# Performance work log

Hardware: AMD Instinct MI355X
Metric: run time of the kernel (lower is better)

## Reference

```python
import jax, jax.numpy as jnp
import numpy as np

NUM_HEADS = 8

def setup_inputs() -> dict:
    key = jax.random.key(0)
    ks = jax.random.split(key, 12)
    B, C, H, W = 4, 256, 64, 64
    QK = 256
    NSP = 256
    x = jax.random.normal(ks[0], (B, C, H, W), dtype=jnp.float32)
    affinity_matrix = jax.random.uniform(ks[1], (B, NSP, H * W), dtype=jnp.float32)
    norm_w = 1.0 + 0.02 * jax.random.normal(ks[2], (C,), dtype=jnp.float32)
    norm_b = 0.02 * jax.random.normal(ks[3], (C,), dtype=jnp.float32)
    Wq = 0.02 * jax.random.normal(ks[4], (QK, C), dtype=jnp.float32)
    Wk = 0.02 * jax.random.normal(ks[5], (QK, C), dtype=jnp.float32)
    Wv = 0.02 * jax.random.normal(ks[6], (C, C), dtype=jnp.float32)
    Wsp = 0.02 * jax.random.normal(ks[7], (QK, C), dtype=jnp.float32)
    lepe_w = 0.02 * jax.random.normal(ks[8], (C, 1, 3, 3), dtype=jnp.float32)  # depthwise OIHW
    lepe_b = 0.02 * jax.random.normal(ks[9], (C,), dtype=jnp.float32)
    return {"x": x, "affinity_matrix": affinity_matrix, "norm_w": norm_w,
            "norm_b": norm_b, "Wq": Wq, "Wk": Wk, "Wv": Wv, "Wsp": Wsp,
            "lepe_w": lepe_w, "lepe_b": lepe_b, "num_spixels": NSP}


def _layernorm2d(x, w, b, eps=1e-6):
    # LayerNorm over channel dim of NCHW input
    xp = x.transpose(0, 2, 3, 1)  # B,H,W,C
    mu = xp.mean(-1, keepdims=True)
    var = ((xp - mu) ** 2).mean(-1, keepdims=True)
    xn = (xp - mu) * jax.lax.rsqrt(var + eps) * w + b
    return xn.transpose(0, 3, 1, 2)


def _sgca(x, affinity_matrix, norm_w, norm_b, Wq, Wk, Wv, Wsp, lepe_w, lepe_b, num_spixels):
    B, C, H, W = x.shape
    HW = H * W
    h = NUM_HEADS
    qk_dim = Wq.shape[0]
    dqk = qk_dim // h
    dv = C // h
    scale = (C // h) ** -0.5

    xn = _layernorm2d(x, norm_w, norm_b)

    # superpixel aggregation: b (hw) c
    x_flat = xn.reshape(B, C, HW).transpose(0, 2, 1)  # B,HW,C
    stoken = jnp.einsum('bmn,bnc->bmc', affinity_matrix, x_flat)
    stoken = stoken / (affinity_matrix.sum(-1, keepdims=True) + 1e-16)  # B,nsp,C

    # sp projection -> B,h,dqk,nsp
    st = jnp.einsum('bmc,qc->bmq', stoken, Wsp).transpose(0, 2, 1)
    st = st.reshape(B, h, dqk, num_spixels)

    # 1x1 conv projections
    q = jnp.einsum('oc,bchw->bohw', Wq, xn).reshape(B, h, dqk, HW)
    k = jnp.einsum('oc,bchw->bohw', Wk, xn).reshape(B, h, dqk, HW)
    vx = jnp.einsum('oc,bchw->bohw', Wv, xn)  # B,C,H,W
    v = vx.reshape(B, h, dv, HW)

    # LePE: depthwise 3x3 conv on v(x)
    lepe = jax.lax.conv_general_dilated(
        vx, lepe_w, window_strides=(1, 1), padding=((1, 1), (1, 1)),
        feature_group_count=C, dimension_numbers=('NCHW', 'OIHW', 'NCHW'))
    lepe = lepe + lepe_b[None, :, None, None]
    # faithful to original: [B,C,HW] -> permute -> [B,HW,C] -> reshape B,C,H,W
    lepe = lepe.reshape(B, C, HW).transpose(0, 2, 1).reshape(B, C, H, W)

    # stage 1: k^T @ stoken, softmax over HW axis
    s_attn = jnp.einsum('bhdn,bhdm->bhnm', k, st) * scale  # B,h,HW,nsp
    s_attn = jax.nn.softmax(s_attn, axis=-2)
    s_out = jnp.einsum('bhdn,bhnm->bhdm', v, s_attn)  # B,h,dv,nsp

    # stage 2: stoken^T @ q, softmax over nsp axis
    x_attn = jnp.einsum('bhdm,bhdn->bhmn', st, q) * scale  # B,h,nsp,HW
    x_attn = jax.nn.softmax(x_attn, axis=-2)
    x_out = jnp.einsum('bhdm,bhmn->bhdn', s_out, x_attn).reshape(B, C, H, W)

    return x_out + lepe


def reference(x, affinity_matrix, norm_w, norm_b, Wq, Wk, Wv, Wsp, lepe_w, lepe_b, num_spixels):
    return _sgca(x, affinity_matrix, norm_w, norm_b, Wq, Wk, Wv, Wsp, lepe_w, lepe_b, num_spixels)
```

## Files before the change

kernel.cpp:

```cpp
#include <hip/hip_runtime.h>
#include <hip/hip_bf16.h>

#define BATCH 4
#define CCH   256
#define HWHW  4096
#define NSP   256
#define NHEAD 8
#define SCALE 0.17677669529663689f
#define PLANE 1048576L

typedef short bf16x8 __attribute__((ext_vector_type(8)));
typedef short bf16x4 __attribute__((ext_vector_type(4)));
typedef float f32x4  __attribute__((ext_vector_type(4)));

__device__ __forceinline__ short f2bs(float f) {
    __hip_bfloat16 h = __float2bfloat16(f);
    return *(short*)&h;
}
__device__ __forceinline__ bf16x8 cvt8(float4 a, float4 b) {
    bf16x8 p;
    p[0] = f2bs(a.x); p[1] = f2bs(a.y); p[2] = f2bs(a.z); p[3] = f2bs(a.w);
    p[4] = f2bs(b.x); p[5] = f2bs(b.y); p[6] = f2bs(b.z); p[7] = f2bs(b.w);
    return p;
}

__global__ __launch_bounds__(512)
void ln_fused_kernel(const float* __restrict__ x, const float* __restrict__ w,
                     const float* __restrict__ bb,
                     const float* __restrict__ Wq, const float* __restrict__ Wk,
                     const float* __restrict__ Wv, const float* __restrict__ Wsp,
                     __hip_bfloat16* __restrict__ xn_cn,
                     __hip_bfloat16* __restrict__ xn_nc,
                     __hip_bfloat16* __restrict__ wbf)
{
    __shared__ float ps[32][64], pss[32][64];
    __shared__ float mus[64], rstds[64];
    __shared__ float wls[256], bls[256];
    int blk = blockIdx.x;
    int t = threadIdx.x;
    if (blk >= 256) {
        int sel = blk - 256;
        const float* src = (sel == 0) ? Wq : (sel == 1) ? Wk : (sel == 2) ? Wv : Wsp;
        __hip_bfloat16* dst = wbf + sel * 65536;
        for (int i = t * 4; i < 65536; i += 2048) {
            float4 f = *(const float4*)(src + i);
            __hip_bfloat16 p[4];
            p[0] = __float2bfloat16(f.x); p[1] = __float2bfloat16(f.y);
            p[2] = __float2bfloat16(f.z); p[3] = __float2bfloat16(f.w);
            *(int2*)(dst + i) = *(int2*)p;
        }
        return;
    }
    int b = blk >> 6;
    int n0 = (blk & 63) * 64;
    int pg = t & 15;
    int cq = t >> 4;
    if (t < 256) { wls[t] = w[t]; bls[t] = bb[t]; }

    const float* xp = x + ((long)(b * CCH + cq * 8)) * HWHW + n0 + pg * 4;
    float4 v[8];
#pragma unroll
    for (int i = 0; i < 8; ++i) v[i] = *(const float4*)(xp + (long)i * HWHW);
    float4 s = {0.f,0.f,0.f,0.f}, ss = {0.f,0.f,0.f,0.f};
#pragma unroll
    for (int i = 0; i < 8; ++i) {
        s.x += v[i].x; s.y += v[i].y; s.z += v[i].z; s.w += v[i].w;
        ss.x += v[i].x * v[i].x; ss.y += v[i].y * v[i].y;
        ss.z += v[i].z * v[i].z; ss.w += v[i].w * v[i].w;
    }
    *(float4*)&ps[cq][pg * 4]  = s;
    *(float4*)&pss[cq][pg * 4] = ss;
    __syncthreads();
    if (t < 64) {
        float S = 0.f, SS = 0.f;
#pragma unroll
        for (int q = 0; q < 32; ++q) { S += ps[q][t]; SS += pss[q][t]; }
        float mu = S * (1.f / 256.f);
        float var = SS * (1.f / 256.f) - mu * mu;
        mus[t] = mu; rstds[t] = rsqrtf(var + 1e-6f);
    }
    __syncthreads();
    float4 mu4 = *(float4*)&mus[pg * 4];
    float4 rs4 = *(float4*)&rstds[pg * 4];

    bf16x8 pk[4];
#pragma unroll
    for (int i = 0; i < 8; ++i) {
        int c = cq * 8 + i;
        float wc = wls[c], bc = bls[c];
        short h0 = f2bs((v[i].x - mu4.x) * rs4.x * wc + bc);
        short h1 = f2bs((v[i].y - mu4.y) * rs4.y * wc + bc);
        short h2 = f2bs((v[i].z - mu4.z) * rs4.z * wc + bc);
        short h3 = f2bs((v[i].w - mu4.w) * rs4.w * wc + bc);
        pk[0][i] = h0; pk[1][i] = h1; pk[2][i] = h2; pk[3][i] = h3;
        bf16x4 q; q[0] = h0; q[1] = h1; q[2] = h2; q[3] = h3;
        *(bf16x4*)(xn_cn + ((long)(b * CCH + c)) * HWHW + n0 + pg * 4) = q;
    }
#pragma unroll
    for (int j = 0; j < 4; ++j)
        *(bf16x8*)(xn_nc + ((long)b * HWHW + n0 + pg * 4 + j) * CCH + cq * 8) = pk[j];
}

template <int OUTK, bool AF32, bool ROWSUM, bool ASUM8>
__device__ __forceinline__ void gemm_body(
    const void* __restrict__ Av, const __hip_bfloat16* __restrict__ B,
    void* __restrict__ Cptr, int bx, int by, int bz,
    int N, int K, int kChunk, int kShift,
    long aStrideZ, long bStrideZ, long cStrideZ,
    float* __restrict__ rsPart,
    __hip_bfloat16* __restrict__ Asm, __hip_bfloat16* __restrict__ Bsm,
    float* __restrict__ rsl)
{
    int z = bz;
    int b = z >> kShift;
    int ch = z & ((1 << kShift) - 1);
    int t = threadIdx.x;
    int lane = t & 63, w = t >> 6;
    int l15 = lane & 15, quad = lane >> 4;
    int Mt = by * 64, Nt = bx * 64;

    if (ASUM8 && t < 64) {
        float s = 0.f;
#pragma unroll
        for (int pl = 0; pl < 8; ++pl) s += rsPart[((b * 8 + pl) << 8) + Mt + t];
        rsl[t] = s;
    }

    long aOff = (long)b * aStrideZ + (long)ch * kChunk
        + (long)(Mt + w * 16 + l15) * K + quad * 8;
    const __hip_bfloat16* aSrcH = (const __hip_bfloat16*)Av + aOff;
    const float*          aSrcF = (const float*)Av + aOff;
    const __hip_bfloat16* bSrc = B + (long)b * bStrideZ + (long)ch * kChunk
        + (long)(Nt + w * 16 + l15) * K + quad * 8;
    __hip_bfloat16* aDst = &Asm[t * 8];
    __hip_bfloat16* bDst = &Bsm[t * 8];

    f32x4 acc00 = {0.f,0.f,0.f,0.f}, acc01 = acc00, acc10 = acc00, acc11 = acc00;
    f32x4 rs0 = acc00, rs1 = acc00;
    bf16x8 onesf;
    { short o = (l15 == 0) ? (short)0x3F80 : (short)0;
      onesf = bf16x8{o, o, o, o, o, o, o, o}; }
    int wm = (w & 1) * 2, wn = (w >> 1) * 2;

    int4 aReg; float4 fA0, fA1;
    if (AF32) { fA0 = *(const float4*)aSrcF; fA1 = *(const float4*)(aSrcF + 4); }
    else if (!ASUM8) aReg = *(const int4*)aSrcH;
    int4 bReg = *(const int4*)bSrc;
    for (int k0 = 0; k0 < kChunk; k0 += 32) {
        if (ASUM8) {
            float4 s0 = {0.f,0.f,0.f,0.f}, s1 = {0.f,0.f,0.f,0.f};
#pragma unroll
            for (int pl = 0; pl < 8; ++pl) {
                const float* p = aSrcF + (long)pl * 65536 + k0;
                float4 u0 = *(const float4*)p, u1 = *(const float4*)(p + 4);
                s0.x += u0.x; s0.y += u0.y; s0.z += u0.z; s0.w += u0.w;
                s1.x += u1.x; s1.y += u1.y; s1.z += u1.z; s1.w += u1.w;
            }
            *(bf16x8*)aDst = cvt8(s0, s1);
        } else if (AF32) *(bf16x8*)aDst = cvt8(fA0, fA1);
        else             *(int4*)aDst = aReg;
        *(int4*)bDst = bReg;
        __syncthreads();
        if (k0 + 32 < kChunk) {
            bSrc += 32;
            bReg = *(const int4*)bSrc;
            if (AF32) { aSrcF += 32; fA0 = *(const float4*)aSrcF; fA1 = *(const float4*)(aSrcF + 4); }
            else if (!ASUM8) { aSrcH += 32; aReg = *(const int4*)aSrcH; }
        }
        bf16x8 a0 = ((const bf16x8*)Asm)[wm * 64 + lane];
        bf16x8 a1 = ((const bf16x8*)Asm)[(wm + 1) * 64 + lane];
        bf16x8 b0 = ((const bf16x8*)Bsm)[wn * 64 + lane];
        bf16x8 b1 = ((const bf16x8*)Bsm)[(wn + 1) * 64 + lane];
        acc00 = __builtin_amdgcn_mfma_f32_16x16x32_bf16(a0, b0, acc00, 0, 0, 0);
        acc01 = __builtin_amdgcn_mfma_f32_16x16x32_bf16(a0, b1, acc01, 0, 0, 0);
        acc10 = __builtin_amdgcn_mfma_f32_16x16x32_bf16(a1, b0, acc10, 0, 0, 0);
        acc11 = __builtin_amdgcn_mfma_f32_16x16x32_bf16(a1, b1, acc11, 0, 0, 0);
        if (ROWSUM) {
            rs0 = __builtin_amdgcn_mfma_f32_16x16x32_bf16(a0, onesf, rs0, 0, 0, 0);
            rs1 = __builtin_amdgcn_mfma_f32_16x16x32_bf16(a1, onesf, rs1, 0, 0, 0);
        }
        __syncthreads();
    }
    if (ROWSUM && bx == 0 && (w >> 1) == 0 && l15 == 0) {
#pragma unroll
        for (int r = 0; r < 4; ++r) {
            rsPart[(long)z * 256 + Mt + wm * 16 + quad * 4 + r]       = rs0[r];
            rsPart[(long)z * 256 + Mt + (wm + 1) * 16 + quad * 4 + r] = rs1[r];
        }
    }
    f32x4 accs[2][2] = {{acc00, acc01}, {acc10, acc11}};
#pragma unroll
    for (int i = 0; i < 2; ++i)
#pragma unroll
        for (int j = 0; j < 2; ++j)
#pragma unroll
            for (int r = 0; r < 4; ++r) {
                int m = Mt + (wm + i) * 16 + quad * 4 + r;
                int n = Nt + (wn + j) * 16 + l15;
                float val = accs[i][j][r];
                if (ASUM8) val /= (rsl[m - Mt] + 1e-16f);
                long off = (long)z * cStrideZ + (long)m * N + n;
                if (OUTK == 0) ((float*)Cptr)[off] = val;
                else ((__hip_bfloat16*)Cptr)[off] = __float2bfloat16(val);
            }
}

__global__ __launch_bounds__(256)
void mega1_kernel(const float* __restrict__ aff,
                  const __hip_bfloat16* __restrict__ xn_cn,
                  const __hip_bfloat16* __restrict__ xn_nc,
                  const __hip_bfloat16* __restrict__ wbf,
                  __hip_bfloat16* __restrict__ qk_nc,
                  __hip_bfloat16* __restrict__ v_cn,
                  float* __restrict__ stoken_part,
                  float* __restrict__ rs_part)
{
    __shared__ __hip_bfloat16 Asm[2048];
    __shared__ __hip_bfloat16 Bsm[2048];
    int blk = blockIdx.x;
    if (blk < 512) {
        int i = blk;
        gemm_body<0, true, true, false>(aff, xn_cn, stoken_part,
            i & 3, (i >> 2) & 3, i >> 4, 256, 4096, 512, 3,
            PLANE, PLANE, 65536L, rs_part, Asm, Bsm, nullptr);
    } else if (blk < 2560) {
        int i = blk - 512;
        gemm_body<1, false, false, false>(xn_nc, wbf, qk_nc,
            i & 7, (i >> 3) & 63, i >> 9, 512, 256, 256, 0,
            PLANE, 0L, 2 * PLANE, nullptr, Asm, Bsm, nullptr);
    } else {
        int i = blk - 2560;
        gemm_body<1, false, false, false>(wbf + 2 * 65536, xn_nc, v_cn,
            i & 63, (i >> 6) & 3, i >> 8, 4096, 256, 256, 0,
            0L, PLANE, PLANE, nullptr, Asm, Bsm, nullptr);
    }
}

__global__ __launch_bounds__(256)
void stmd_kernel(const float* __restrict__ part,
                 const __hip_bfloat16* __restrict__ wsp,
                 __hip_bfloat16* __restrict__ st_md,
                 float* __restrict__ rs_part)
{
    __shared__ __hip_bfloat16 Asm[2048];
    __shared__ __hip_bfloat16 Bsm[2048];
    __shared__ float rsl[64];
    int i = blockIdx.x;
    gemm_body<1, false, false, true>(part, wsp, st_md,
        i & 3, (i >> 2) & 3, i >> 4, 256, 256, 256, 0,
        524288L, 0L, 65536L, rs_part, Asm, Bsm, rsl);
}

__device__ __forceinline__
void stage1_dev(char* smem, int chunk, int bh,
                const __hip_bfloat16* __restrict__ qk_nc,
                const __hip_bfloat16* __restrict__ v_cn,
                const __hip_bfloat16* __restrict__ st_md,
                __hip_bfloat16* __restrict__ opart)
{
    __hip_bfloat16* Es  = (__hip_bfloat16*)smem;
    __hip_bfloat16* sts = (__hip_bfloat16*)(smem + 36864);
    const int b = bh >> 3, h = bh & 7;
    const int t = threadIdx.x, lane = t & 63, w = t >> 6;
    const int l15 = lane & 15, quad = lane >> 4;
    const int n0 = chunk * 256;

    {
        const int4* src = (const int4*)(st_md + ((long)(b * 256 + t)) * 256 + h * 32);
        int4* dst = (int4*)&sts[t * 40];
        dst[0] = src[0]; dst[1] = src[1]; dst[2] = src[2]; dst[3] = src[3];
    }
    __syncthreads();
    bf16x8 afrag[16];
#pragma unroll
    for (int mt = 0; mt < 16; ++mt)
        afrag[mt] = *(const bf16x8*)&sts[(mt * 16 + l15) * 40 + quad * 8];
    bf16x8 onesf;
    { short o = (l15 == 0) ? (short)0x3F80 : (short)0;
      onesf = bf16x8{o, o, o, o, o, o, o, o}; }

    f32x4 occ[4][3];
#pragma unroll
    for (int i = 0; i < 4; ++i)
#pragma unroll
        for (int j = 0; j < 3; ++j) occ[i][j] = f32x4{0.f,0.f,0.f,0.f};

    for (int sub = 0; sub < 4; ++sub) {
        const int nbase = n0 + sub * 64;
        bf16x8 kf = *(const bf16x8*)(qk_nc + ((long)b * 4096 + nbase + 16 * w + l15) * 512 + 256 + h * 32 + quad * 8);
#pragma unroll
        for (int mt = 0; mt < 16; ++mt) {
            f32x4 s = __builtin_amdgcn_mfma_f32_16x16x32_bf16(afrag[mt], kf, f32x4{0.f,0.f,0.f,0.f}, 0, 0, 0);
#pragma unroll
            for (int r = 0; r < 4; ++r)
                Es[(mt * 16 + quad * 4 + r) * 72 + 16 * w + l15] =
                    __float2bfloat16(__expf(s[r] * SCALE));
        }
        __syncthreads();
#pragma unroll
        for (int ks = 0; ks < 2; ++ks) {
            bf16x8 bf0 = *(const bf16x8*)(v_cn + ((long)(b * 256 + h * 32 + l15)) * 4096 + nbase + ks * 32 + quad * 8);
            bf16x8 bf1 = *(const bf16x8*)(v_cn + ((long)(b * 256 + h * 32 + 16 + l15)) * 4096 + nbase + ks * 32 + quad * 8);
#pragma unroll
            for (int mi = 0; mi < 4; ++mi) {
                bf16x8 af = *(const bf16x8*)&Es[(64 * w + mi * 16 + l15) * 72 + ks * 32 + quad * 8];
                occ[mi][0] = __builtin_amdgcn_mfma_f32_16x16x32_bf16(af, bf0, occ[mi][0], 0, 0, 0);
                occ[mi][1] = __builtin_amdgcn_mfma_f32_16x16x32_bf16(af, bf1, occ[mi][1], 0, 0, 0);
                occ[mi][2] = __builtin_amdgcn_mfma_f32_16x16x32_bf16(af, onesf, occ[mi][2], 0, 0, 0);
            }
        }
        __syncthreads();
    }
    __hip_bfloat16* tb = Es;
#pragma unroll
    for (int mi = 0; mi < 4; ++mi)
#pragma unroll
        for (int jt = 0; jt < 3; ++jt) {
            if (jt == 2 && l15 != 0) continue;
            int col = jt * 16 + l15;
#pragma unroll
            for (int r = 0; r < 4; ++r) {
                int m = 64 * w + mi * 16 + quad * 4 + r;
                tb[col * 264 + m] = __float2bfloat16(occ[mi][jt][r]);
            }
        }
    __syncthreads();
    int* og = (int*)(opart) + (long)(chunk * 32 + bh) * 4224;
    const int* tbi = (const int*)tb;
#pragma unroll
    for (int i = 0; i < 17; ++i) {
        int idx = t + i * 256;
        if (idx < 4224) {
            int row = idx >> 7, off = idx & 127;
            og[idx] = tbi[row * 132 + off];
        }
    }
}

__device__ __forceinline__
void lepe_dev(char* smem, int bx, int cy, int b,
              const __hip_bfloat16* __restrict__ v_cn,
              const float* __restrict__ lw, const float* __restrict__ lb,
              __hip_bfloat16* __restrict__ lepe_cn)
{
    __hip_bfloat16* in_t    = (__hip_bfloat16*)smem;
    __hip_bfloat16* tile_bf = (__hip_bfloat16*)(smem + 24576);
    float* wls = (float*)(smem + 41472);
    float* bls = (float*)(smem + 42624);
    const int c0 = cy * 32;
    const int t = threadIdx.x;
    const int n0 = bx * 256, r0 = bx * 4;

    for (int i = t; i < 288; i += 256) wls[i] = lw[c0 * 9 + i];
    if (t < 32)  bls[t] = lb[c0 + t];
#pragma unroll
    for (int i = 0; i < 6; ++i) {
        int vi = t + i * 256;
        int ch = vi / 48;
        int off = (vi % 48) * 8;
        int g = (r0 - 1) * 64 + off;
        int4 val = {0, 0, 0, 0};
        if ((unsigned)g < 4096u)
            val = *(const int4*)(v_cn + (((long)(b * CCH + c0 + ch)) << 12) + g);
        *(int4*)&in_t[ch * 384 + off] = val;
    }
    __syncthreads();

    const int lane = t & 63, w = t >> 6;
#pragma unroll
    for (int i = 0; i < 8; ++i) {
        int ch = w * 8 + i;
        float cr[6], lf[6], rf[6];
#pragma unroll
        for (int rr = 0; rr < 6; ++rr) {
            cr[rr] = (float)in_t[ch * 384 + rr * 64 + lane];
            float lv = __shfl_up(cr[rr], 1);
            float rv = __shfl_down(cr[rr], 1);
            lf[rr] = (lane == 0) ? 0.f : lv;
            rf[rr] = (lane == 63) ? 0.f : rv;
        }
        float w0 = wls[ch*9+0], w1 = wls[ch*9+1], w2 = wls[ch*9+2];
        float w3 = wls[ch*9+3], w4 = wls[ch*9+4], w5 = wls[ch*9+5];
        float w6 = wls[ch*9+6], w7 = wls[ch*9+7], w8 = wls[ch*9+8];
        float bias = bls[ch];
#pragma unroll
        for (int r = 0; r < 4; ++r) {
            float acc = bias
                + lf[r]   * w0 + cr[r]   * w1 + rf[r]   * w2
                + lf[r+1] * w3 + cr[r+1] * w4 + rf[r+1] * w5
                + lf[r+2] * w6 + cr[r+2] * w7 + rf[r+2] * w8;
            tile_bf[(r * 64 + lane) * 33 + ch] = __float2bfloat16(acc);
        }
    }
    __syncthreads();
#pragma unroll
    for (int i = 0; i < 32; ++i) {
        int idx = t + i * 256;
        int nl = idx >> 5, cj = idx & 31;
        int sp = n0 + nl;
        lepe_cn[((long)(b * CCH + (sp >> 4)) << 12) + (nl & 15) * 256 + c0 + cj] =
            tile_bf[nl * 33 + cj];
    }
}

__global__ __launch_bounds__(256)
void mega2_kernel(const __hip_bfloat16* __restrict__ qk_nc,
                  const __hip_bfloat16* __restrict__ v_cn,
                  const __hip_bfloat16* __restrict__ st_md,
                  __hip_bfloat16* __restrict__ opart,
                  const float* __restrict__ lw, const float* __restrict__ lb,
                  __hip_bfloat16* __restrict__ lepe_cn)
{
    __shared__ __align__(16) char smem[57344];
    int blk = blockIdx.x;
    if (blk < 512) {
        stage1_dev(smem, blk & 15, blk >> 4, qk_nc, v_cn, st_md, opart);
    } else {
        int j = blk - 512;
        lepe_dev(smem, j & 15, (j >> 4) & 7, j >> 7, v_cn, lw, lb, lepe_cn);
    }
}

__global__ __launch_bounds__(256)
void merge1_kernel(const __hip_bfloat16* __restrict__ opart, __hip_bfloat16* __restrict__ sout)
{
    int t = blockIdx.x * 256 + threadIdx.x;
    int m = t & 255;
    int d = (t >> 8) & 31;
    int bh = t >> 13;
    float num = 0.f, den = 0.f;
    for (int ch = 0; ch < 16; ++ch) {
        long base = (long)((ch * 32 + bh) * 33) * 256 + m;
        num += (float)opart[base + (long)d * 256];
        den += (float)opart[base + 32 * 256];
    }
    sout[(long)bh * 8192 + d * 256 + m] = __float2bfloat16(num / den);
}

__global__ __launch_bounds__(256)
void stage2_mfma(const __hip_bfloat16* __restrict__ qk_nc,
                 const __hip_bfloat16* __restrict__ st_md,
                 const __hip_bfloat16* __restrict__ sout_bf,
                 const __hip_bfloat16* __restrict__ lepe_cn,
                 float* __restrict__ out)
{
    __shared__ __hip_bfloat16 Es2[64 * 264];
    __shared__ __hip_bfloat16 sts[256 * 40];
    __shared__ __hip_bfloat16 sos[32 * 264];
    __shared__ float o_t[32 * 68];
    const int chunk = blockIdx.x, bh = blockIdx.y;
    const int b = bh >> 3, h = bh & 7;
    const int t = threadIdx.x, lane = t & 63, w = t >> 6;
    const int l15 = lane & 15, quad = lane >> 4;
    const int n0 = chunk * 256;

    {
        const int4* src = (const int4*)(st_md + ((long)(b * 256 + t)) * 256 + h * 32);
        int4* dst = (int4*)&sts[t * 40];
        dst[0] = src[0]; dst[1] = src[1]; dst[2] = src[2]; dst[3] = src[3];
    }
    {
        int row = t >> 3, seg = t & 7;
        const int4* src = (const int4*)(sout_bf + (long)bh * 8192 + row * 256 + seg * 32);
        int4* dst = (int4*)&sos[row * 264 + seg * 32];
        dst[0] = src[0]; dst[1] = src[1]; dst[2] = src[2]; dst[3] = src[3];
    }
    __syncthreads();
    bf16x8 stfrag[4];
#pragma unroll
    for (int mt = 0; mt < 4; ++mt)
        stfrag[mt] = *(const bf16x8*)&sts[(64 * w + mt * 16 + l15) * 40 + quad * 8];
    bf16x8 onesf;
    { short o = (l15 == 0) ? (short)0x3F80 : (short)0;
      onesf = bf16x8{o, o, o, o, o, o, o, o}; }

    for (int sub = 0; sub < 4; ++sub) {
        const int nbase = n0 + sub * 64;
#pragma unroll
        for (int nt = 0; nt < 4; ++nt) {
            bf16x8 qf = *(const bf16x8*)(qk_nc + ((long)b * 4096 + nbase + nt * 16 + l15) * 512 + h * 32 + quad * 8);
#pragma unroll
            for (int mt = 0; mt < 4; ++mt) {
                f32x4 s = __builtin_amdgcn_mfma_f32_16x16x32_bf16(qf, stfrag[mt], f32x4{0.f,0.f,0.f,0.f}, 0, 0, 0);
#pragma unroll
                for (int r = 0; r < 4; ++r)
                    Es2[(nt * 16 + quad * 4 + r) * 264 + 64 * w + mt * 16 + l15] =
                        __float2bfloat16(__expf(s[r] * SCALE));
            }
        }
        __syncthreads();
        f32x4 o0 = {0.f,0.f,0.f,0.f}, o1 = o0, o2 = o0;
#pragma unroll
        for (int ks = 0; ks < 8; ++ks) {
            bf16x8 af = *(const bf16x8*)&Es2[(16 * w + l15) * 264 + ks * 32 + quad * 8];
            bf16x8 b0 = *(const bf16x8*)&sos[(l15) * 264 + ks * 32 + quad * 8];
            bf16x8 b1 = *(const bf16x8*)&sos[(16 + l15) * 264 + ks * 32 + quad * 8];
            o0 = __builtin_amdgcn_mfma_f32_16x16x32_bf16(af, b0, o0, 0, 0, 0);
            o1 = __builtin_amdgcn_mfma_f32_16x16x32_bf16(af, b1, o1, 0, 0, 0);
            o2 = __builtin_amdgcn_mfma_f32_16x16x32_bf16(af, onesf, o2, 0, 0, 0);
        }
        __syncthreads();
#pragma unroll
        for (int r = 0; r < 4; ++r) {
            float den = __shfl(o2[r], lane & 48);
            float inv = 1.f / den;
            o_t[(l15) * 68 + 16 * w + quad * 4 + r]      = o0[r] * inv;
            o_t[(16 + l15) * 68 + 16 * w + quad * 4 + r] = o1[r] * inv;
        }
        __syncthreads();
        {
            int row = t >> 3, coff = (t & 7) * 8;
            long gb = ((long)(b * 256 + h * 32 + row)) * 4096 + nbase + coff;
            int4 lp4 = *(const int4*)(lepe_cn + gb);
            const __hip_bfloat16* lp = (const __hip_bfloat16*)&lp4;
            const float* sp = &o_t[row * 68 + coff];
            float4 r0, r1;
            r0.x = sp[0] + (float)lp[0]; r0.y = sp[1] + (float)lp[1];
            r0.z = sp[2] + (float)lp[2]; r0.w = sp[3] + (float)lp[3];
            r1.x = sp[4] + (float)lp[4]; r1.y = sp[5] + (float)lp[5];
            r1.z = sp[6] + (float)lp[6]; r1.w = sp[7] + (float)lp[7];
            *(float4*)(out + gb)     = r0;
            *(float4*)(out + gb + 4) = r1;
        }
        __syncthreads();
    }
}

extern "C" void kernel_launch(void* const* d_in, const int* in_sizes, int n_in,
                              void* d_out, int out_size, void* d_ws, size_t ws_size,
                              hipStream_t stream)
{
    const float* x    = (const float*)d_in[0];
    const float* aff  = (const float*)d_in[1];
    const float* nw   = (const float*)d_in[2];
    const float* nb   = (const float*)d_in[3];
    const float* Wq   = (const float*)d_in[4];
    const float* Wk   = (const float*)d_in[5];
    const float* Wv   = (const float*)d_in[6];
    const float* Wsp  = (const float*)d_in[7];
    const float* lw   = (const float*)d_in[8];
    const float* lb   = (const float*)d_in[9];
    float* out = (float*)d_out;

    float* ws = (float*)d_ws;
    const long P = PLANE;
    __hip_bfloat16* qk_nc  = (__hip_bfloat16*)(ws);
    __hip_bfloat16* v_cn   = (__hip_bfloat16*)(ws + 4 * P);
    __hip_bfloat16* xn_cn  = (__hip_bfloat16*)(ws + 6 * P);
    __hip_bfloat16* xn_nc  = (__hip_bfloat16*)(ws + 8 * P);
    __hip_bfloat16* lepe_cn= (__hip_bfloat16*)(ws + 10 * P);
    float* stoken_part = ws + 14 * P;
    __hip_bfloat16* opart = (__hip_bfloat16*)(ws + 16 * P);
    float* tail        = ws + 16 * P + 2162688;
    __hip_bfloat16* wbf       = (__hip_bfloat16*)tail;
    __hip_bfloat16* st_md     = (__hip_bfloat16*)(tail + 262144);
    __hip_bfloat16* sout_bf   = (__hip_bfloat16*)(tail + 393216);
    float* rs_part = tail + 525312;

    ln_fused_kernel<<<260, 512, 0, stream>>>(x, nw, nb, Wq, Wk, Wv, Wsp,
                                             xn_cn, xn_nc, wbf);
    mega1_kernel<<<3584, 256, 0, stream>>>(aff, xn_cn, xn_nc, wbf,
                                           qk_nc, v_cn, stoken_part, rs_part);
    stmd_kernel<<<64, 256, 0, stream>>>(stoken_part, wbf + 3 * 65536, st_md, rs_part);
    mega2_kernel<<<1024, 256, 0, stream>>>(qk_nc, v_cn, st_md, opart, lw, lb, lepe_cn);
    merge1_kernel<<<1024, 256, 0, stream>>>(opart, sout_bf);
    stage2_mfma<<<dim3(16, 32), 256, 0, stream>>>(qk_nc, st_md, sout_bf, lepe_cn, out);
}
```

Measured before the change: 212.3 us.

## Widen GEMM tiles, use direct global-to-LDS loads, double K step

The shared GEMM body now processes 64 K elements per barrier pair instead of 32, and loads bf16 operands with global_load_lds so they bypass registers. The affinity-aggregation GEMM now has each block compute four 64-column tiles (NTL=4), which reuses the fp32-to-bf16 converted affinity rows and cuts its block count from 512 to 128. The aim is fewer barriers, less register staging and less redundant conversion of the affinity matrix. In exchange LDS use per block rises to about 40 KB and the affinity GEMM has far fewer blocks, which may lower occupancy and parallelism.

After: 208.0 us. 1.02x faster.

```diff
diff --git a/kernel.cpp b/kernel.cpp
--- a/kernel.cpp
+++ b/kernel.cpp
@@ -22,6 +22,12 @@
     p[0] = f2bs(a.x); p[1] = f2bs(a.y); p[2] = f2bs(a.z); p[3] = f2bs(a.w);
     p[4] = f2bs(b.x); p[5] = f2bs(b.y); p[6] = f2bs(b.z); p[7] = f2bs(b.w);
     return p;
+}
+__device__ __forceinline__ void gll16(const __hip_bfloat16* g, __hip_bfloat16* l) {
+    __builtin_amdgcn_global_load_lds(
+        (const __attribute__((address_space(1))) unsigned int*)(const void*)g,
+        (__attribute__((address_space(3))) unsigned int*)(void*)l,
+        16, 0, 0);
 }
 
 __global__ __launch_bounds__(512)
@@ -101,7 +107,7 @@
         *(bf16x8*)(xn_nc + ((long)b * HWHW + n0 + pg * 4 + j) * CCH + cq * 8) = pk[j];
 }
 
-template <int OUTK, bool AF32, bool ROWSUM, bool ASUM8>
+template <int OUTK, int ASTAGE, bool ROWSUM, int NTL>
 __device__ __forceinline__ void gemm_body(
     const void* __restrict__ Av, const __hip_bfloat16* __restrict__ B,
     void* __restrict__ Cptr, int bx, int by, int bz,
@@ -117,9 +123,9 @@
     int t = threadIdx.x;
     int lane = t & 63, w = t >> 6;
     int l15 = lane & 15, quad = lane >> 4;
-    int Mt = by * 64, Nt = bx * 64;
-
-    if (ASUM8 && t < 64) {
+    int Mt = by * 64, Nt = bx * 64 * NTL;
+
+    if (ASTAGE == 2 && t < 64) {
         float s = 0.f;
 #pragma unroll
         for (int pl = 0; pl < 8; ++pl) s += rsPart[((b * 8 + pl) << 8) + Mt + t];
@@ -132,52 +138,78 @@
     const float*          aSrcF = (const float*)Av + aOff;
     const __hip_bfloat16* bSrc = B + (long)b * bStrideZ + (long)ch * kChunk
         + (long)(Nt + w * 16 + l15) * K + quad * 8;
-    __hip_bfloat16* aDst = &Asm[t * 8];
-    __hip_bfloat16* bDst = &Bsm[t * 8];
-
-    f32x4 acc00 = {0.f,0.f,0.f,0.f}, acc01 = acc00, acc10 = acc00, acc11 = acc00;
-    f32x4 rs0 = acc00, rs1 = acc00;
+
+    f32x4 acc[NTL][2][2];
+#pragma unroll
+    for (int nt = 0; nt < NTL; ++nt)
+#pragma unroll
+        for (int i = 0; i < 2; ++i)
+#pragma unroll
+            for (int j = 0; j < 2; ++j) acc[nt][i][j] = f32x4{0.f,0.f,0.f,0.f};
+    f32x4 rs0 = {0.f,0.f,0.f,0.f}, rs1 = rs0;
     bf16x8 onesf;
     { short o = (l15 == 0) ? (short)0x3F80 : (short)0;
       onesf = bf16x8{o, o, o, o, o, o, o, o}; }
     int wm = (w & 1) * 2, wn = (w >> 1) * 2;
 
-    int4 aReg; float4 fA0, fA1;
-    if (AF32) { fA0 = *(const float4*)aSrcF; fA1 = *(const float4*)(aSrcF + 4); }
-    else if (!ASUM8) aReg = *(const int4*)aSrcH;
-    int4 bReg = *(const int4*)bSrc;
-    for (int k0 = 0; k0 < kChunk; k0 += 32) {
-        if (ASUM8) {
-            float4 s0 = {0.f,0.f,0.f,0.f}, s1 = {0.f,0.f,0.f,0.f};
-#pragma unroll
-            for (int pl = 0; pl < 8; ++pl) {
-                const float* p = aSrcF + (long)pl * 65536 + k0;
-                float4 u0 = *(const float4*)p, u1 = *(const float4*)(p + 4);
-                s0.x += u0.x; s0.y += u0.y; s0.z += u0.z; s0.w += u0.w;
-                s1.x += u1.x; s1.y += u1.y; s1.z += u1.z; s1.w += u1.w;
+    float4 pf0, pf1, pf2, pf3;
+    if (ASTAGE == 1) {
+        pf0 = *(const float4*)(aSrcF);      pf1 = *(const float4*)(aSrcF + 4);
+        pf2 = *(const float4*)(aSrcF + 32); pf3 = *(const float4*)(aSrcF + 36);
+    }
+
+    const bf16x8* AsmU = (const bf16x8*)Asm;
+    const bf16x8* BsmU = (const bf16x8*)Bsm;
+
+    for (int k0 = 0; k0 < kChunk; k0 += 64) {
+        if (ASTAGE == 0) {
+            gll16(aSrcH + k0,      Asm + w * 512);
+            gll16(aSrcH + k0 + 32, Asm + 2048 + w * 512);
+        } else if (ASTAGE == 1) {
+            *(bf16x8*)&Asm[t * 8]        = cvt8(pf0, pf1);
+            *(bf16x8*)&Asm[2048 + t * 8] = cvt8(pf2, pf3);
+        } else {
+#pragma unroll
+            for (int kh = 0; kh < 2; ++kh) {
+                float4 s0 = {0.f,0.f,0.f,0.f}, s1 = {0.f,0.f,0.f,0.f};
+#pragma unroll
+                for (int pl = 0; pl < 8; ++pl) {
+                    const float* p = aSrcF + (long)pl * 65536 + k0 + kh * 32;
+                    float4 u0 = *(const float4*)p, u1 = *(const float4*)(p + 4);
+                    s0.x += u0.x; s0.y += u0.y; s0.z += u0.z; s0.w += u0.w;
+                    s1.x += u1.x; s1.y += u1.y; s1.z += u1.z; s1.w += u1.w;
+                }
+                *(bf16x8*)&Asm[kh * 2048 + t * 8] = cvt8(s0, s1);
             }
-            *(bf16x8*)aDst = cvt8(s0, s1);
-        } else if (AF32) *(bf16x8*)aDst = cvt8(fA0, fA1);
-        else             *(int4*)aDst = aReg;
-        *(int4*)bDst = bReg;
-        __syncthreads();
-        if (k0 + 32 < kChunk) {
-            bSrc += 32;
-            bReg = *(const int4*)bSrc;
-            if (AF32) { aSrcF += 32; fA0 = *(const float4*)aSrcF; fA1 = *(const float4*)(aSrcF + 4); }
-            else if (!ASUM8) { aSrcH += 32; aReg = *(const int4*)aSrcH; }
-        }
-        bf16x8 a0 = ((const bf16x8*)Asm)[wm * 64 + lane];
-        bf16x8 a1 = ((const bf16x8*)Asm)[(wm + 1) * 64 + lane];
-        bf16x8 b0 = ((const bf16x8*)Bsm)[wn * 64 + lane];
-        bf16x8 b1 = ((const bf16x8*)Bsm)[(wn + 1) * 64 + lane];
-        acc00 = __builtin_amdgcn_mfma_f32_16x16x32_bf16(a0, b0, acc00, 0, 0, 0);
-        acc01 = __builtin_amdgcn_mfma_f32_16x16x32_bf16(a0, b1, acc01, 0, 0, 0);
-        acc10 = __builtin_amdgcn_mfma_f32_16x16x32_bf16(a1, b0, acc10, 0, 0, 0);
-        acc11 = __builtin_amdgcn_mfma_f32_16x16x32_bf16(a1, b1, acc11, 0, 0, 0);
-        if (ROWSUM) {
-            rs0 = __builtin_amdgcn_mfma_f32_16x16x32_bf16(a0, onesf, rs0, 0, 0, 0);
-            rs1 = __builtin_amdgcn_mfma_f32_16x16x32_bf16(a1, onesf, rs1, 0, 0, 0);
+        }
+#pragma unroll
+        for (int nt = 0; nt < NTL; ++nt) {
+            gll16(bSrc + (long)nt * 64 * K + k0,      Bsm + nt * 4096 + w * 512);
+            gll16(bSrc + (long)nt * 64 * K + k0 + 32, Bsm + nt * 4096 + 2048 + w * 512);
+        }
+        __syncthreads();
+        if (ASTAGE == 1 && k0 + 64 < kChunk) {
+            const float* nx = aSrcF + k0 + 64;
+            pf0 = *(const float4*)nx;        pf1 = *(const float4*)(nx + 4);
+            pf2 = *(const float4*)(nx + 32); pf3 = *(const float4*)(nx + 36);
+        }
+#pragma unroll
+        for (int kh = 0; kh < 2; ++kh) {
+            bf16x8 a0 = AsmU[kh * 256 + wm * 64 + lane];
+            bf16x8 a1 = AsmU[kh * 256 + (wm + 1) * 64 + lane];
+            if (ROWSUM) {
+                rs0 = __builtin_amdgcn_mfma_f32_16x16x32_bf16(a0, onesf, rs0, 0, 0, 0);
+                rs1 = __builtin_amdgcn_mfma_f32_16x16x32_bf16(a1, onesf, rs1, 0, 0, 0);
+            }
+#pragma unroll
+            for (int nt = 0; nt < NTL; ++nt) {
+                bf16x8 b0 = BsmU[nt * 512 + kh * 256 + wn * 64 + lane];
+                bf16x8 b1 = BsmU[nt * 512 + kh * 256 + (wn + 1) * 64 + lane];
+                acc[nt][0][0] = __builtin_amdgcn_mfma_f32_16x16x32_bf16(a0, b0, acc[nt][0][0], 0, 0, 0);
+                acc[nt][0][1] = __builtin_amdgcn_mfma_f32_16x16x32_bf16(a0, b1, acc[nt][0][1], 0, 0, 0);
+                acc[nt][1][0] = __builtin_amdgcn_mfma_f32_16x16x32_bf16(a1, b0, acc[nt][1][0], 0, 0, 0);
+                acc[nt][1][1] = __builtin_amdgcn_mfma_f32_16x16x32_bf16(a1, b1, acc[nt][1][1], 0, 0, 0);
+            }
         }
         __syncthreads();
     }
@@ -188,21 +220,22 @@
             rsPart[(long)z * 256 + Mt + (wm + 1) * 16 + quad * 4 + r] = rs1[r];
         }
     }
-    f32x4 accs[2][2] = {{acc00, acc01}, {acc10, acc11}};
-#pragma unroll
-    for (int i = 0; i < 2; ++i)
-#pragma unroll
-        for (int j = 0; j < 2; ++j)
-#pragma unroll
-            for (int r = 0; r < 4; ++r) {
-                int m = Mt + (wm + i) * 16 + quad * 4 + r;
-                int n = Nt + (wn + j) * 16 + l15;
-                float val = accs[i][j][r];
-                if (ASUM8) val /= (rsl[m - Mt] + 1e-16f);
-                long off = (long)z * cStrideZ + (long)m * N + n;
-                if (OUTK == 0) ((float*)Cptr)[off] = val;
-                else ((__hip_bfloat16*)Cptr)[off] = __float2bfloat16(val);
-            }
+#pragma unroll
+    for (int nt = 0; nt < NTL; ++nt)
+#pragma unroll
+        for (int i = 0; i < 2; ++i)
+#pragma unroll
+            for (int j = 0; j < 2; ++j)
+#pragma unroll
+                for (int r = 0; r < 4; ++r) {
+                    int m = Mt + (wm + i) * 16 + quad * 4 + r;
+                    int n = Nt + nt * 64 + (wn + j) * 16 + l15;
+                    float val = acc[nt][i][j][r];
+                    if (ASTAGE == 2) val /= (rsl[m - Mt] + 1e-16f);
+                    long off = (long)z * cStrideZ + (long)m * N + n;
+                    if (OUTK == 0) ((float*)Cptr)[off] = val;
+                    else ((__hip_bfloat16*)Cptr)[off] = __float2bfloat16(val);
+                }
 }
 
 __global__ __launch_bounds__(256)
@@ -215,22 +248,22 @@
                   float* __restrict__ stoken_part,
                   float* __restrict__ rs_part)
 {
-    __shared__ __hip_bfloat16 Asm[2048];
-    __shared__ __hip_bfloat16 Bsm[2048];
+    __shared__ __hip_bfloat16 Asm[4096];
+    __shared__ __hip_bfloat16 Bsm[4 * 4096];
     int blk = blockIdx.x;
-    if (blk < 512) {
+    if (blk < 128) {
         int i = blk;
-        gemm_body<0, true, true, false>(aff, xn_cn, stoken_part,
-            i & 3, (i >> 2) & 3, i >> 4, 256, 4096, 512, 3,
+        gemm_body<0, 1, true, 4>(aff, xn_cn, stoken_part,
+            0, i & 3, i >> 2, 256, 4096, 512, 3,
             PLANE, PLANE, 65536L, rs_part, Asm, Bsm, nullptr);
-    } else if (blk < 2560) {
-        int i = blk - 512;
-        gemm_body<1, false, false, false>(xn_nc, wbf, qk_nc,
+    } else if (blk < 2176) {
+        int i = blk - 128;
+        gemm_body<1, 0, false, 1>(xn_nc, wbf, qk_nc,
             i & 7, (i >> 3) & 63, i >> 9, 512, 256, 256, 0,
             PLANE, 0L, 2 * PLANE, nullptr, Asm, Bsm, nullptr);
     } else {
-        int i = blk - 2560;
-        gemm_body<1, false, false, false>(wbf + 2 * 65536, xn_nc, v_cn,
+        int i = blk - 2176;
+        gemm_body<1, 0, false, 1>(wbf + 2 * 65536, xn_nc, v_cn,
             i & 63, (i >> 6) & 3, i >> 8, 4096, 256, 256, 0,
             0L, PLANE, PLANE, nullptr, Asm, Bsm, nullptr);
     }
@@ -242,11 +275,11 @@
                  __hip_bfloat16* __restrict__ st_md,
                  float* __restrict__ rs_part)
 {
-    __shared__ __hip_bfloat16 Asm[2048];
-    __shared__ __hip_bfloat16 Bsm[2048];
+    __shared__ __hip_bfloat16 Asm[4096];
+    __shared__ __hip_bfloat16 Bsm[4096];
     __shared__ float rsl[64];
     int i = blockIdx.x;
-    gemm_body<1, false, false, true>(part, wsp, st_md,
+    gemm_body<1, 2, false, 1>(part, wsp, st_md,
         i & 3, (i >> 2) & 3, i >> 4, 256, 256, 256, 0,
         524288L, 0L, 65536L, rs_part, Asm, Bsm, rsl);
 }
@@ -559,7 +592,7 @@
 
     ln_fused_kernel<<<260, 512, 0, stream>>>(x, nw, nb, Wq, Wk, Wv, Wsp,
                                              xn_cn, xn_nc, wbf);
-    mega1_kernel<<<3584, 256, 0, stream>>>(aff, xn_cn, xn_nc, wbf,
+    mega1_kernel<<<3200, 256, 0, stream>>>(aff, xn_cn, xn_nc, wbf,
                                            qk_nc, v_cn, stoken_part, rs_part);
     stmd_kernel<<<64, 256, 0, stream>>>(stoken_part, wbf + 3 * 65536, st_md, rs_part);
     mega2_kernel<<<1024, 256, 0, stream>>>(qk_nc, v_cn, st_md, opart, lw, lb, lepe_cn);
```
